# Performance work log

Hardware: AMD Instinct MI355X
Metric: run time of the kernel (lower is better)

The kernel has to match this reference:

```python
import jax, jax.numpy as jnp
import numpy as np

N_IN = 2_000_000
N_OUT = 250_000
K = 8          # 2x2x2 octree kernel, stride 2
C_IN = 32
C_OUT = 64
BN_EPS = 1e-5


def setup_inputs() -> dict:
    key = jax.random.key(0)
    k1, k2, k3, k4, k5 = jax.random.split(key, 5)
    data = jax.random.normal(k1, (N_IN, C_IN), dtype=jnp.float32)
    # Octree neighbor table: index of each of the 8 children of every output
    # octant; -1 marks an empty child (nempty=True).
    neigh = jax.random.randint(k2, (N_OUT, K), 0, N_IN, dtype=jnp.int32)
    empty = jax.random.uniform(k3, (N_OUT, K)) < 0.2
    neigh = jnp.where(empty, -1, neigh)
    # Conv weight [K*C_IN, C_OUT] + bias, BatchNorm affine params.
    scale = 1.0 / np.sqrt(K * C_IN)
    weight = jax.random.normal(k4, (K * C_IN, C_OUT), dtype=jnp.float32) * scale
    bias = jnp.zeros((C_OUT,), dtype=jnp.float32)
    gamma = jnp.ones((C_OUT,), dtype=jnp.float32)
    beta = jnp.zeros((C_OUT,), dtype=jnp.float32)
    return {"data": data, "weight": weight, "bias": bias,
            "gamma": gamma, "beta": beta, "neigh": neigh}


def reference(data, weight, bias, gamma, beta, neigh):
    # --- OctreeConv stride-2, kernel 2x2x2, nempty=True ---
    valid = (neigh >= 0)                               # [N_OUT, K]
    idx = jnp.where(valid, neigh, 0)
    gathered = data[idx] * valid[..., None].astype(data.dtype)  # [N_OUT, K, C_IN]
    out = gathered.reshape(gathered.shape[0], -1) @ weight + bias  # [N_OUT, C_OUT]
    # --- BatchNorm1d (training: batch stats, biased variance) ---
    mean = jnp.mean(out, axis=0)
    var = jnp.var(out, axis=0)
    out = (out - mean) * jax.lax.rsqrt(var + BN_EPS) * gamma + beta
    return out
```

## Files before the change

### kernel.cpp

```cpp
#include <hip/hip_runtime.h>
#include <hip/hip_bf16.h>

#define C_INC   32
#define C_OUTC  64
#define KNBR    8
#define BN_EPS  1e-5f

#define BT_STRIDE 264
#define NB_PAD 1024

typedef __bf16 bf16x8 __attribute__((ext_vector_type(8)));
typedef float  floatx4 __attribute__((ext_vector_type(4)));

__device__ inline unsigned short f2bf_bits(float f) {
    unsigned int u = __builtin_bit_cast(unsigned int, f);
    unsigned int r = (u + 0x7FFFu + ((u >> 16) & 1u)) >> 16;
    return (unsigned short)r;
}
__device__ inline __bf16 f2bf(float f) {
    return __builtin_bit_cast(__bf16, f2bf_bits(f));
}

__global__ __launch_bounds__(256) void conv_kernel(
    const float* __restrict__ data,
    const float* __restrict__ weight,
    const float* __restrict__ bias,
    const int*   __restrict__ neigh,
    float*       __restrict__ out,
    float*       __restrict__ partialsT,
    int n_out)
{
    __shared__ unsigned short Bt[C_OUTC * BT_STRIDE];
    __shared__ float red[2 * C_OUTC];

    const int t    = threadIdx.x;
    const int lane = t & 63;
    const int wave = t >> 6;
    const int m16  = lane & 15;
    const int q    = lane >> 4;

    if (t < 2 * C_OUTC) red[t] = 0.0f;

    {
        const int n = t & 63;
        const int g = t >> 6;
        #pragma unroll 8
        for (int kk = 0; kk < 64; ++kk) {
            int k = kk * 4 + g;
            Bt[n * BT_STRIDE + k] = f2bf_bits(weight[k * C_OUTC + n]);
        }
    }
    __syncthreads();

    float biasv[4];
    #pragma unroll
    for (int nt = 0; nt < 4; ++nt) biasv[nt] = bias[nt * 16 + m16];

    float s1[4] = {0.f, 0.f, 0.f, 0.f};
    float s2[4] = {0.f, 0.f, 0.f, 0.f};

    const int rowBase = blockIdx.x * 256;
    const int4* __restrict__ neigh4 = reinterpret_cast<const int4*>(neigh);

    for (int pass = 0; pass < 4; ++pass) {
        const int tile0 = rowBase + pass * 64 + wave * 16;
        if (tile0 >= n_out) continue;

        floatx4 acc[4];
        #pragma unroll
        for (int nt = 0; nt < 4; ++nt) acc[nt] = (floatx4){0.f, 0.f, 0.f, 0.f};

        const int arow = tile0 + m16;

        const int4 nA = neigh4[(size_t)arow * 2 + 0];
        const int4 nB = neigh4[(size_t)arow * 2 + 1];
        int nidxs[KNBR] = {nA.x, nA.y, nA.z, nA.w, nB.x, nB.y, nB.z, nB.w};

        float4 g0[KNBR], g1[KNBR];
        #pragma unroll
        for (int ks = 0; ks < KNBR; ++ks) {
            g0[ks] = (float4){0.f, 0.f, 0.f, 0.f};
            g1[ks] = (float4){0.f, 0.f, 0.f, 0.f};
            if (nidxs[ks] >= 0) {
                const float4* p = reinterpret_cast<const float4*>(
                    data + (size_t)nidxs[ks] * C_INC + q * 8);
                g0[ks] = p[0];
                g1[ks] = p[1];
            }
        }

        #pragma unroll
        for (int ks = 0; ks < KNBR; ++ks) {
            bf16x8 a;
            a[0] = f2bf(g0[ks].x); a[1] = f2bf(g0[ks].y);
            a[2] = f2bf(g0[ks].z); a[3] = f2bf(g0[ks].w);
            a[4] = f2bf(g1[ks].x); a[5] = f2bf(g1[ks].y);
            a[6] = f2bf(g1[ks].z); a[7] = f2bf(g1[ks].w);

            #pragma unroll
            for (int nt = 0; nt < 4; ++nt) {
                const bf16x8 b = *reinterpret_cast<const bf16x8*>(
                    &Bt[(nt * 16 + m16) * BT_STRIDE + ks * 32 + q * 8]);
                acc[nt] = __builtin_amdgcn_mfma_f32_16x16x32_bf16(a, b, acc[nt], 0, 0, 0);
            }
        }

        #pragma unroll
        for (int nt = 0; nt < 4; ++nt) {
            const int c = nt * 16 + m16;
            #pragma unroll
            for (int r = 0; r < 4; ++r) {
                const int drow = tile0 + q * 4 + r;
                const float v = acc[nt][r] + biasv[nt];
                out[(size_t)drow * C_OUTC + c] = v;
                s1[nt] += v;
                s2[nt] += v * v;
            }
        }
    }

    #pragma unroll
    for (int nt = 0; nt < 4; ++nt) {
        #pragma unroll
        for (int off = 16; off < 64; off <<= 1) {
            s1[nt] += __shfl_xor(s1[nt], off, 64);
            s2[nt] += __shfl_xor(s2[nt], off, 64);
        }
    }
    if (q == 0) {
        #pragma unroll
        for (int nt = 0; nt < 4; ++nt) {
            const int c = nt * 16 + m16;
            atomicAdd(&red[c], s1[nt]);
            atomicAdd(&red[C_OUTC + c], s2[nt]);
        }
    }
    __syncthreads();
    if (t < 2 * C_OUTC) {
        partialsT[(size_t)t * NB_PAD + blockIdx.x] = red[t];
    }
}

__global__ __launch_bounds__(256) void stats_kernel(
    const float* __restrict__ partialsT, int nb,
    const float* __restrict__ gamma, const float* __restrict__ beta,
    float* __restrict__ ab, int n_out)
{
    const int t    = threadIdx.x;
    const int lane = t & 63;
    const int wave = t >> 6;
    const int c    = blockIdx.x;

    float sA = 0.f, sB = 0.f;
    for (int b = t; b < nb; b += 256) {
        sA += partialsT[(size_t)c * NB_PAD + b];
        sB += partialsT[(size_t)(C_OUTC + c) * NB_PAD + b];
    }
    #pragma unroll
    for (int off = 1; off < 64; off <<= 1) {
        sA += __shfl_xor(sA, off, 64);
        sB += __shfl_xor(sB, off, 64);
    }
    __shared__ float red[8];
    if (lane == 0) { red[wave] = sA; red[4 + wave] = sB; }
    __syncthreads();
    if (t == 0) {
        const float S1 = (red[0] + red[1]) + (red[2] + red[3]);
        const float S2 = (red[4] + red[5]) + (red[6] + red[7]);
        const float invN = 1.0f / (float)n_out;
        const float mean = S1 * invN;
        const float var  = S2 * invN - mean * mean;
        const float rstd = rsqrtf(var + BN_EPS);
        const float a    = gamma[c] * rstd;
        ab[c]          = a;
        ab[C_OUTC + c] = beta[c] - mean * a;
    }
}

__global__ __launch_bounds__(256) void bn_kernel(
    float* __restrict__ out, const float* __restrict__ ab, long n4)
{
    const long i = (long)blockIdx.x * blockDim.x + threadIdx.x;
    if (i >= n4) return;
    const int c4 = (int)(i & 15);
    float4 v = reinterpret_cast<float4*>(out)[i];
    const float4 a  = reinterpret_cast<const float4*>(ab)[c4];
    const float4 bb = reinterpret_cast<const float4*>(ab + C_OUTC)[c4];
    v.x = v.x * a.x + bb.x;
    v.y = v.y * a.y + bb.y;
    v.z = v.z * a.z + bb.z;
    v.w = v.w * a.w + bb.w;
    reinterpret_cast<float4*>(out)[i] = v;
}

extern "C" void kernel_launch(void* const* d_in, const int* in_sizes, int n_in,
                              void* d_out, int out_size, void* d_ws, size_t ws_size,
                              hipStream_t stream) {
    const float* data   = (const float*)d_in[0];
    const float* weight = (const float*)d_in[1];
    const float* bias   = (const float*)d_in[2];
    const float* gamma  = (const float*)d_in[3];
    const float* beta   = (const float*)d_in[4];
    const int*   neigh  = (const int*)d_in[5];

    const int n_out = in_sizes[5] / KNBR;
    float* out = (float*)d_out;

    const int nb = (n_out + 255) / 256;

    float* partialsT = (float*)d_ws;
    float* ab = partialsT + (size_t)128 * NB_PAD;

    hipLaunchKernelGGL(conv_kernel, dim3(nb), dim3(256), 0, stream,
                       data, weight, bias, neigh, out, partialsT, n_out);
    hipLaunchKernelGGL(stats_kernel, dim3(C_OUTC), dim3(256), 0, stream,
                       partialsT, nb, gamma, beta, ab, n_out);
    const long n4 = (long)n_out * C_OUTC / 4;
    hipLaunchKernelGGL(bn_kernel, dim3((unsigned)((n4 + 255) / 256)), dim3(256), 0, stream,
                       out, ab, n4);
}
```

Baseline: 380.5 us.

## Swizzle weight LDS layout, prefetch neighbor indices, and fuse gather with MFMA

The padded weight tile in LDS is replaced with an XOR-swizzled 256-stride layout, and the block-reduction buffer now reuses that LDS, so shared memory per block shrinks. Launch bounds ask for 5 blocks per SM. The neighbor indices for the next pass are prefetched while the current pass computes. The per-neighbor gather is folded into the MFMA loop so all 16 float4 gathers no longer sit in registers at once. Together these aim to raise occupancy and hide gather latency, at the cost of fewer gathers in flight per wave and possible register pressure or spills under the tighter bound.

```diff
diff --git a/kernel.cpp b/kernel.cpp
--- a/kernel.cpp
+++ b/kernel.cpp
@@ -6,7 +6,6 @@
 #define KNBR    8
 #define BN_EPS  1e-5f
 
-#define BT_STRIDE 264
 #define NB_PAD 1024
 
 typedef __bf16 bf16x8 __attribute__((ext_vector_type(8)));
@@ -21,7 +20,11 @@
     return __builtin_bit_cast(__bf16, f2bf_bits(f));
 }
 
-__global__ __launch_bounds__(256) void conv_kernel(
+__device__ inline int bt_off(int n, int k) {
+    return n * 256 + ((((k >> 3) ^ (n & 7)) << 3) | (k & 7));
+}
+
+__global__ __launch_bounds__(256, 5) void conv_kernel(
     const float* __restrict__ data,
     const float* __restrict__ weight,
     const float* __restrict__ bias,
@@ -30,16 +33,13 @@
     float*       __restrict__ partialsT,
     int n_out)
 {
-    __shared__ unsigned short Bt[C_OUTC * BT_STRIDE];
-    __shared__ float red[2 * C_OUTC];
+    __shared__ unsigned short Bt[C_OUTC * 256];
 
     const int t    = threadIdx.x;
     const int lane = t & 63;
     const int wave = t >> 6;
     const int m16  = lane & 15;
     const int q    = lane >> 4;
-
-    if (t < 2 * C_OUTC) red[t] = 0.0f;
 
     {
         const int n = t & 63;
@@ -47,7 +47,7 @@
         #pragma unroll 8
         for (int kk = 0; kk < 64; ++kk) {
             int k = kk * 4 + g;
-            Bt[n * BT_STRIDE + k] = f2bf_bits(weight[k * C_OUTC + n]);
+            Bt[bt_off(n, k)] = f2bf_bits(weight[k * C_OUTC + n]);
         }
     }
     __syncthreads();
@@ -62,61 +62,79 @@
     const int rowBase = blockIdx.x * 256;
     const int4* __restrict__ neigh4 = reinterpret_cast<const int4*>(neigh);
 
+    int4 nA = {-1, -1, -1, -1}, nB = {-1, -1, -1, -1};
+    {
+        const int tile0 = rowBase + wave * 16;
+        if (tile0 < n_out) {
+            const int arow = tile0 + m16;
+            nA = neigh4[(size_t)arow * 2 + 0];
+            nB = neigh4[(size_t)arow * 2 + 1];
+        }
+    }
+
+    #pragma unroll
     for (int pass = 0; pass < 4; ++pass) {
         const int tile0 = rowBase + pass * 64 + wave * 16;
-        if (tile0 >= n_out) continue;
-
-        floatx4 acc[4];
-        #pragma unroll
-        for (int nt = 0; nt < 4; ++nt) acc[nt] = (floatx4){0.f, 0.f, 0.f, 0.f};
-
-        const int arow = tile0 + m16;
-
-        const int4 nA = neigh4[(size_t)arow * 2 + 0];
-        const int4 nB = neigh4[(size_t)arow * 2 + 1];
-        int nidxs[KNBR] = {nA.x, nA.y, nA.z, nA.w, nB.x, nB.y, nB.z, nB.w};
-
-        float4 g0[KNBR], g1[KNBR];
-        #pragma unroll
-        for (int ks = 0; ks < KNBR; ++ks) {
-            g0[ks] = (float4){0.f, 0.f, 0.f, 0.f};
-            g1[ks] = (float4){0.f, 0.f, 0.f, 0.f};
-            if (nidxs[ks] >= 0) {
-                const float4* p = reinterpret_cast<const float4*>(
-                    data + (size_t)nidxs[ks] * C_INC + q * 8);
-                g0[ks] = p[0];
-                g1[ks] = p[1];
+        const bool valid = (tile0 < n_out);
+
+        int4 mA = {-1, -1, -1, -1}, mB = {-1, -1, -1, -1};
+        if (pass < 3) {
+            const int ntile0 = rowBase + (pass + 1) * 64 + wave * 16;
+            if (ntile0 < n_out) {
+                const int narow = ntile0 + m16;
+                mA = neigh4[(size_t)narow * 2 + 0];
+                mB = neigh4[(size_t)narow * 2 + 1];
             }
         }
 
-        #pragma unroll
-        for (int ks = 0; ks < KNBR; ++ks) {
-            bf16x8 a;
-            a[0] = f2bf(g0[ks].x); a[1] = f2bf(g0[ks].y);
-            a[2] = f2bf(g0[ks].z); a[3] = f2bf(g0[ks].w);
-            a[4] = f2bf(g1[ks].x); a[5] = f2bf(g1[ks].y);
-            a[6] = f2bf(g1[ks].z); a[7] = f2bf(g1[ks].w);
+        if (valid) {
+            floatx4 acc[4];
+            #pragma unroll
+            for (int nt = 0; nt < 4; ++nt) acc[nt] = (floatx4){0.f, 0.f, 0.f, 0.f};
+
+            const int nidxs[KNBR] = {nA.x, nA.y, nA.z, nA.w,
+                                     nB.x, nB.y, nB.z, nB.w};
+
+            #pragma unroll
+            for (int ks = 0; ks < KNBR; ++ks) {
+                float4 f0 = {0.f, 0.f, 0.f, 0.f};
+                float4 f1 = {0.f, 0.f, 0.f, 0.f};
+                if (nidxs[ks] >= 0) {
+                    const float4* p = reinterpret_cast<const float4*>(
+                        data + (size_t)nidxs[ks] * C_INC + q * 8);
+                    f0 = p[0];
+                    f1 = p[1];
+                }
+                bf16x8 a;
+                a[0] = f2bf(f0.x); a[1] = f2bf(f0.y);
+                a[2] = f2bf(f0.z); a[3] = f2bf(f0.w);
+                a[4] = f2bf(f1.x); a[5] = f2bf(f1.y);
+                a[6] = f2bf(f1.z); a[7] = f2bf(f1.w);
+
+                #pragma unroll
+                for (int nt = 0; nt < 4; ++nt) {
+                    const bf16x8 b = *reinterpret_cast<const bf16x8*>(
+                        &Bt[bt_off(nt * 16 + m16, ks * 32 + q * 8)]);
+                    acc[nt] = __builtin_amdgcn_mfma_f32_16x16x32_bf16(a, b, acc[nt], 0, 0, 0);
+                }
+            }
 
             #pragma unroll
             for (int nt = 0; nt < 4; ++nt) {
-                const bf16x8 b = *reinterpret_cast<const bf16x8*>(
-                    &Bt[(nt * 16 + m16) * BT_STRIDE + ks * 32 + q * 8]);
-                acc[nt] = __builtin_amdgcn_mfma_f32_16x16x32_bf16(a, b, acc[nt], 0, 0, 0);
+                const int c = nt * 16 + m16;
+                #pragma unroll
+                for (int r = 0; r < 4; ++r) {
+                    const int drow = tile0 + q * 4 + r;
+                    const float v = acc[nt][r] + biasv[nt];
+                    out[(size_t)drow * C_OUTC + c] = v;
+                    s1[nt] += v;
+                    s2[nt] += v * v;
+                }
             }
         }
 
-        #pragma unroll
-        for (int nt = 0; nt < 4; ++nt) {
-            const int c = nt * 16 + m16;
-            #pragma unroll
-            for (int r = 0; r < 4; ++r) {
-                const int drow = tile0 + q * 4 + r;
-                const float v = acc[nt][r] + biasv[nt];
-                out[(size_t)drow * C_OUTC + c] = v;
-                s1[nt] += v;
-                s2[nt] += v * v;
-            }
-        }
+        nA = mA;
+        nB = mB;
     }
 
     #pragma unroll
@@ -127,17 +145,22 @@
             s2[nt] += __shfl_xor(s2[nt], off, 64);
         }
     }
+
+    __syncthreads();
+    float* redf = reinterpret_cast<float*>(Bt);
+    if (t < 2 * C_OUTC) redf[t] = 0.0f;
+    __syncthreads();
     if (q == 0) {
         #pragma unroll
         for (int nt = 0; nt < 4; ++nt) {
             const int c = nt * 16 + m16;
-            atomicAdd(&red[c], s1[nt]);
-            atomicAdd(&red[C_OUTC + c], s2[nt]);
+            atomicAdd(&redf[c], s1[nt]);
+            atomicAdd(&redf[C_OUTC + c], s2[nt]);
         }
     }
     __syncthreads();
     if (t < 2 * C_OUTC) {
-        partialsT[(size_t)t * NB_PAD + blockIdx.x] = red[t];
+        partialsT[(size_t)t * NB_PAD + blockIdx.x] = redf[t];
     }
 }
 
```

Result: no change. 381.3 us (+0.2%).
